# Performance work log

Hardware: AMD Instinct MI355X
Metric: run time of the kernel (lower is better)

## Reference

```python
import jax, jax.numpy as jnp
import numpy as np
import math

D_MODEL = 1024
DIM_K = 1024
DIM_V = 1024
N_HEADS = 16
B, T = 4, 1024


def setup_inputs() -> dict:
    key = jax.random.key(0)
    ks = jax.random.split(key, 12)
    s = 1.0 / math.sqrt(D_MODEL)
    inp = {
        "x": jax.random.normal(ks[0], (B, T, D_MODEL), jnp.float32),
        "mask": jax.random.randint(ks[1], (T, T), 0, 2, jnp.int32),
        "adj": jax.random.normal(ks[2], (T, T), jnp.float32) * 0.1,
        "Wq": jax.random.normal(ks[3], (D_MODEL, DIM_K), jnp.float32) * s,
        "bq": jnp.zeros((DIM_K,), jnp.float32),
        "Wk": jax.random.normal(ks[4], (D_MODEL, DIM_K), jnp.float32) * s,
        "bk": jnp.zeros((DIM_K,), jnp.float32),
        "Wv": jax.random.normal(ks[5], (D_MODEL, DIM_V), jnp.float32) * s,
        "bv": jnp.zeros((DIM_V,), jnp.float32),
        "Wo": jax.random.normal(ks[6], (DIM_V, D_MODEL), jnp.float32) * (1.0 / math.sqrt(DIM_V)),
        "bo": jnp.zeros((D_MODEL,), jnp.float32),
        "alpha": jnp.asarray(0.0, jnp.float32),
        "n_heads": N_HEADS,
    }
    return inp


def reference(x, mask, adj, Wq, bq, Wk, bk, Wv, bv, Wo, bo, alpha, n_heads):
    b, t, d = x.shape
    dim_k = Wq.shape[1]
    dim_v = Wv.shape[1]
    dkh = dim_k // n_heads
    dvh = dim_v // n_heads
    norm_fact = 1.0 / math.sqrt(dim_k)

    # torch .view(-1, B, T, dkh): plain row-major reshape with heads leading
    Q = (x @ Wq + bq).reshape(n_heads, b, t, dkh)
    K = (x @ Wk + bk).reshape(n_heads, b, t, dkh)
    V = (x @ Wv + bv).reshape(n_heads, b, t, dvh)

    # shared score computation [H, B, T, T]
    g_map = jnp.einsum("hbqd,hbkd->hbqk", Q, K) * norm_fact + adj
    l_map = jnp.where(mask == 0, jnp.asarray(-1e9, g_map.dtype), g_map)

    g_att = jax.nn.softmax(g_map, axis=-1)
    l_att = jax.nn.softmax(l_map, axis=-1)

    x_g = jnp.einsum("hbqk,hbkd->hbqd", g_att, V).reshape(b, t, -1)
    x_l = jnp.einsum("hbqk,hbkd->hbqd", l_att, V).reshape(b, t, -1)

    a = jax.nn.sigmoid(alpha)
    x_o = a * x_g + (1.0 - a) * x_l

    # signed sqrt + L2 normalize (norm=True)
    x_o = jnp.sqrt(jax.nn.relu(x_o)) - jnp.sqrt(jax.nn.relu(-x_o))
    x_o = x_o / jnp.maximum(jnp.linalg.norm(x_o, axis=-1, keepdims=True), 1e-12)

    return (x_o @ Wo + bo).reshape(-1, t, d)
```

## Files before the change

kernel.cpp:

```cpp
#include <hip/hip_runtime.h>
#include <hip/hip_bf16.h>


typedef __attribute__((ext_vector_type(8))) short short8;
typedef __attribute__((ext_vector_type(4))) float f32x4;
typedef __attribute__((ext_vector_type(2))) int i32x2;

__device__ __forceinline__ f32x4 mfma16(short8 a, short8 b, f32x4 c) {
  return __builtin_amdgcn_mfma_f32_16x16x32_bf16(a, b, c, 0, 0, 0);
}

__device__ __forceinline__ unsigned short f2b(float f) {
  __hip_bfloat16 h = __float2bfloat16(f);
  return *reinterpret_cast<unsigned short*>(&h);
}

__device__ __forceinline__ unsigned cvtpk(float lo, float hi) {
  unsigned r;
  asm("v_cvt_pk_bf16_f32 %0, %1, %2" : "=v"(r) : "v"(lo), "v"(hi));
  return r;
}

__device__ __forceinline__ float exp2h(float x) {
  float r;
  asm("v_exp_f32 %0, %1" : "=v"(r) : "v"(x));
  return r;
}

__device__ __forceinline__ unsigned ldsoff(const void* p) {
  return (unsigned)(size_t)(const __attribute__((address_space(3))) char*)p;
}

template <int OFF>
__device__ __forceinline__ i32x2 dstr(unsigned addr) {
  i32x2 d;
  asm volatile("ds_read_b64_tr_b16 %0, %1 offset:%c2"
               : "=v"(d) : "v"(addr), "i"(OFF) : "memory");
  return d;
}

__device__ __forceinline__ void gload_lds16(const void* g, void* l) {
  __builtin_amdgcn_global_load_lds(
      (const __attribute__((address_space(1))) void*)g,
      (__attribute__((address_space(3))) void*)l, 16, 0, 0);
}

__global__ __launch_bounds__(256) void k_cast_x(const float* __restrict__ x,
                                                unsigned short* __restrict__ xb) {
  int i = (blockIdx.x * 256 + threadIdx.x) * 8;
  float4 a = *reinterpret_cast<const float4*>(x + i);
  float4 b = *reinterpret_cast<const float4*>(x + i + 4);
  short8 o;
  o[0] = (short)f2b(a.x); o[1] = (short)f2b(a.y);
  o[2] = (short)f2b(a.z); o[3] = (short)f2b(a.w);
  o[4] = (short)f2b(b.x); o[5] = (short)f2b(b.y);
  o[6] = (short)f2b(b.z); o[7] = (short)f2b(b.w);
  *reinterpret_cast<short8*>(xb + i) = o;
}

__global__ __launch_bounds__(256) void k_transW(const float* __restrict__ Wq,
                                                const float* __restrict__ Wk,
                                                const float* __restrict__ Wv,
                                                const float* __restrict__ Wo,
                                                unsigned short* __restrict__ WcatT,
                                                unsigned short* __restrict__ WoT) {
  int wsel = blockIdx.z;
  const float* src = wsel == 0 ? Wq : wsel == 1 ? Wk : wsel == 2 ? Wv : Wo;
  unsigned short* dst = (wsel < 3) ? (WcatT + (size_t)wsel * 1024 * 1024) : WoT;
  int k0 = blockIdx.x * 64, n0 = blockIdx.y * 64;
  __shared__ float tile[64][65];
  int tr = threadIdx.x >> 6, tc = threadIdx.x & 63;
#pragma unroll
  for (int i = 0; i < 16; ++i) {
    int r = i * 4 + tr;
    tile[r][tc] = src[(size_t)(k0 + r) * 1024 + n0 + tc];
  }
  __syncthreads();
#pragma unroll
  for (int i = 0; i < 16; ++i) {
    int r = i * 4 + tr;
    dst[(size_t)(n0 + r) * 1024 + k0 + tc] = f2b(tile[tc][r]);
  }
}

__global__ __launch_bounds__(256) void k_pack(const float* __restrict__ adj,
                                              const int* __restrict__ mask,
                                              unsigned int* __restrict__ AM) {
  const float L2E = 1.4426950408889634f;
  int i = (blockIdx.x * 256 + threadIdx.x) * 4;
  int q = i >> 10, c = i & 1023;
  float4 a = *reinterpret_cast<const float4*>(adj + i);
  int4 m = *reinterpret_cast<const int4*>(mask + i);
  unsigned B = (unsigned)(q * 1024) + ((c >> 6) * 64) + ((c & 15) * 4) + ((c >> 4) & 3);
  AM[B]      = ((unsigned)f2b(a.x * L2E) << 16) | (m.x != 0 ? 1u : 0u);
  AM[B + 4]  = ((unsigned)f2b(a.y * L2E) << 16) | (m.y != 0 ? 1u : 0u);
  AM[B + 8]  = ((unsigned)f2b(a.z * L2E) << 16) | (m.z != 0 ? 1u : 0u);
  AM[B + 12] = ((unsigned)f2b(a.w * L2E) << 16) | (m.w != 0 ? 1u : 0u);
}

template <int MODE>
__global__ __launch_bounds__(256) void k_gemm(
    const unsigned short* __restrict__ A, const unsigned short* __restrict__ BT,
    float* __restrict__ outF,
    unsigned short* __restrict__ oQ, unsigned short* __restrict__ oK,
    unsigned short* __restrict__ oV,
    const float* __restrict__ b0, const float* __restrict__ b1,
    const float* __restrict__ b2, int M, int N, int K) {
  __shared__ unsigned short As[128 * 32], Bs[128 * 32];
  const int tid = threadIdx.x;
  const int w = tid >> 6, l = tid & 63, l15 = l & 15, l4 = l >> 4;
  const int m0 = blockIdx.x * 128, n0 = blockIdx.y * 128;
  const int wm = (w >> 1) * 64, wn = (w & 1) * 64;
  f32x4 acc[4][4];
#pragma unroll
  for (int i = 0; i < 4; ++i)
#pragma unroll
    for (int j = 0; j < 4; ++j) acc[i][j] = f32x4{0.f, 0.f, 0.f, 0.f};

  const int nkt = K >> 5;
  for (int kt = 0; kt < nkt; ++kt) {
#pragma unroll
    for (int i = 0; i < 2; ++i) {
      int c = i * 256 + tid;
      gload_lds16(A + (size_t)(m0 + (c >> 2)) * K + kt * 32 + (c & 3) * 8,
                  (char*)As + c * 16);
      gload_lds16(BT + (size_t)(n0 + (c >> 2)) * K + kt * 32 + (c & 3) * 8,
                  (char*)Bs + c * 16);
    }
    __syncthreads();
    short8 af[4], bf[4];
#pragma unroll
    for (int i = 0; i < 4; ++i)
      af[i] = *reinterpret_cast<const short8*>(As + (wm + i * 16 + l15) * 32 + l4 * 8);
#pragma unroll
    for (int j = 0; j < 4; ++j)
      bf[j] = *reinterpret_cast<const short8*>(Bs + (wn + j * 16 + l15) * 32 + l4 * 8);
#pragma unroll
    for (int i = 0; i < 4; ++i)
#pragma unroll
      for (int j = 0; j < 4; ++j) acc[i][j] = mfma16(af[i], bf[j], acc[i][j]);
    __syncthreads();
  }
#pragma unroll
  for (int i = 0; i < 4; ++i)
#pragma unroll
    for (int j = 0; j < 4; ++j) {
      int gr0 = m0 + wm + i * 16 + l4 * 4;
      int gc = n0 + wn + j * 16 + l15;
      if (MODE == 0) {
        int mat = gc >> 10, nl = gc & 1023;
        const float* bp = mat == 0 ? b0 : mat == 1 ? b1 : b2;
        unsigned short* op = mat == 0 ? oQ : mat == 1 ? oK : oV;
        float bb = bp[nl];
#pragma unroll
        for (int r = 0; r < 4; ++r)
          op[(size_t)(gr0 + r) * 1024 + nl] = f2b(acc[i][j][r] + bb);
      } else {
        float bb = b0[gc];
#pragma unroll
        for (int r = 0; r < 4; ++r)
          outF[(size_t)(gr0 + r) * N + gc] = acc[i][j][r] + bb;
      }
    }
}

__global__ __launch_bounds__(256) void k_attn(
    const unsigned short* __restrict__ Qb, const unsigned short* __restrict__ Kb,
    const unsigned short* __restrict__ Vb, const unsigned int* __restrict__ AM,
    float* __restrict__ Xg, float* __restrict__ Xl) {
  const int g = blockIdx.x;
  const int q0 = blockIdx.y * 64;
  const int tid = threadIdx.x;
  const int w = tid >> 6, l = tid & 63, l15 = l & 15, l4 = l >> 4;

  __shared__ unsigned short Kt[2][2][64][32];
  __shared__ unsigned short Vs[2][4][64][16];
  __shared__ unsigned short Pt[4][2][64][16];

  const size_t gbase = (size_t)g << 16;
  const unsigned short* Qg = Qb + gbase;
  const unsigned short* Kg = Kb + gbase;
  const unsigned short* Vg = Vb + gbase;

  short8 qf[2];
  {
    const unsigned short* qp = Qg + (size_t)(q0 + w * 16 + l15) * 64 + l4 * 8;
    qf[0] = *reinterpret_cast<const short8*>(qp);
    qf[1] = *reinterpret_cast<const short8*>(qp + 32);
  }
  short8 onesf;
#pragma unroll
  for (int j = 0; j < 8; ++j) onesf[j] = (short)0x3F80;

  f32x4 accg[4], accl[4];
#pragma unroll
  for (int d = 0; d < 4; ++d) {
    accg[d] = f32x4{0.f, 0.f, 0.f, 0.f};
    accl[d] = f32x4{0.f, 0.f, 0.f, 0.f};
  }
  f32x4 sumg = f32x4{0.f, 0.f, 0.f, 0.f}, suml = f32x4{0.f, 0.f, 0.f, 0.f};

  const int qrow = q0 + w * 16 + l4 * 4;
  const float NF2 = 0.04508422002778f;
  const uint4* AMr4 = (const uint4*)AM;
  const int kx8 = (l4 ^ ((l15 >> 1) & 3)) * 8;

  const unsigned ptw = ldsoff(&Pt[w][0][0][0]) + (unsigned)(l4 * 256 + l15 * 8);
  const unsigned vsb = ldsoff(&Vs[0][0][0][0]) + (unsigned)(l4 * 256 + l15 * 8);

  auto stage = [&](int b, int kk0) {
#pragma unroll
    for (int i = 0; i < 2; ++i) {
      int c = i * 256 + tid;
      int dk = c >> 8, key = (c >> 2) & 63, slot = c & 3;
      int ls = slot ^ ((key >> 1) & 3);
      gload_lds16(Kg + (size_t)(kk0 + key) * 64 + dk * 32 + ls * 8,
                  (char*)Kt + b * 8192 + c * 16);
    }
#pragma unroll
    for (int i = 0; i < 2; ++i) {
      int c = i * 256 + tid;
      int db = c >> 7, k = (c >> 1) & 63, h = c & 1;
      gload_lds16(Vg + (size_t)(kk0 + k) * 64 + db * 16 + h * 8,
                  (char*)Vs + b * 8192 + c * 16);
    }
  };

  stage(0, 0);
  __syncthreads();

  for (int kt = 0; kt < 16; ++kt) {
    const int b = kt & 1;
    if (kt < 15) stage(b ^ 1, (kt + 1) * 64);

    union { uint4 v; unsigned u[4]; } amu[4];
#pragma unroll
    for (int r = 0; r < 4; ++r)
      amu[r].v = AMr4[(size_t)(qrow + r) * 256 + kt * 16 + l15];

    f32x4 accs[4];
#pragma unroll
    for (int cb = 0; cb < 4; ++cb) accs[cb] = f32x4{0.f, 0.f, 0.f, 0.f};
#pragma unroll
    for (int cb = 0; cb < 4; ++cb)
#pragma unroll
      for (int dk = 0; dk < 2; ++dk)
        accs[cb] = mfma16(
            qf[dk],
            *reinterpret_cast<const short8*>(&Kt[b][dk][cb * 16 + l15][kx8]),
            accs[cb]);

#pragma unroll
    for (int cb = 0; cb < 4; ++cb) {
      unsigned am0 = amu[0].u[cb], am1 = amu[1].u[cb];
      unsigned am2 = amu[2].u[cb], am3 = amu[3].u[cb];
      float e0 = exp2h(fmaf(accs[cb][0], NF2, __uint_as_float(am0 & 0xffff0000u)));
      float e1 = exp2h(fmaf(accs[cb][1], NF2, __uint_as_float(am1 & 0xffff0000u)));
      float e2 = exp2h(fmaf(accs[cb][2], NF2, __uint_as_float(am2 & 0xffff0000u)));
      float e3 = exp2h(fmaf(accs[cb][3], NF2, __uint_as_float(am3 & 0xffff0000u)));
      float z0 = (am0 & 1u) ? e0 : 0.f;
      float z1 = (am1 & 1u) ? e1 : 0.f;
      float z2 = (am2 & 1u) ? e2 : 0.f;
      float z3 = (am3 & 1u) ? e3 : 0.f;
      int krow = cb * 16 + l15;
      *reinterpret_cast<uint2*>(&Pt[w][0][krow][l4 * 4]) =
          make_uint2(cvtpk(e0, e1), cvtpk(e2, e3));
      *reinterpret_cast<uint2*>(&Pt[w][1][krow][l4 * 4]) =
          make_uint2(cvtpk(z0, z1), cvtpk(z2, z3));
    }
    asm volatile("s_waitcnt lgkmcnt(0)" ::: "memory");

    const unsigned vb = vsb + (unsigned)(b << 13);
#pragma unroll
    for (int ks = 0; ks < 2; ++ks) {
      union { short8 s; i32x2 d[2]; } vf[4], pg, pl;
      if (ks == 0) {
#pragma unroll
        for (int db = 0; db < 4; ++db) {
          vf[db].d[0] = dstr<0 * 1024 + 0>(vb + db * 2048);
          vf[db].d[1] = dstr<0 * 1024 + 128>(vb + db * 2048);
        }
        pg.d[0] = dstr<0>(ptw);        pg.d[1] = dstr<128>(ptw);
        pl.d[0] = dstr<2048>(ptw);     pl.d[1] = dstr<2048 + 128>(ptw);
      } else {
#pragma unroll
        for (int db = 0; db < 4; ++db) {
          vf[db].d[0] = dstr<1 * 1024 + 0>(vb + db * 2048);
          vf[db].d[1] = dstr<1 * 1024 + 128>(vb + db * 2048);
        }
        pg.d[0] = dstr<1024>(ptw);     pg.d[1] = dstr<1024 + 128>(ptw);
        pl.d[0] = dstr<2048 + 1024>(ptw);
        pl.d[1] = dstr<2048 + 1024 + 128>(ptw);
      }
      asm volatile("s_waitcnt lgkmcnt(0)" ::: "memory");
      __builtin_amdgcn_sched_barrier(0);
#pragma unroll
      for (int db = 0; db < 4; ++db) {
        accg[db] = mfma16(pg.s, vf[db].s, accg[db]);
        accl[db] = mfma16(pl.s, vf[db].s, accl[db]);
      }
      sumg = mfma16(pg.s, onesf, sumg);
      suml = mfma16(pl.s, onesf, suml);
    }
    __syncthreads();
  }

#pragma unroll
  for (int r = 0; r < 4; ++r) {
    float ig = 1.f / sumg[r];
    float il = suml[r] > 0.f ? 1.f / suml[r] : 0.f;
#pragma unroll
    for (int db = 0; db < 4; ++db) {
      size_t o = gbase + (size_t)(qrow + r) * 64 + db * 16 + l15;
      Xg[o] = accg[db][r] * ig;
      Xl[o] = accl[db][r] * il;
    }
  }
}

__global__ __launch_bounds__(256) void k_combine(const float* __restrict__ Xg,
                                                 const float* __restrict__ Xl,
                                                 const float* __restrict__ alphap,
                                                 unsigned short* __restrict__ xob) {
  int row = blockIdx.x, tid = threadIdx.x;
  int w = tid >> 6, l = tid & 63;
  size_t base = (size_t)row * 1024 + tid * 4;
  float a = 1.f / (1.f + __expf(-alphap[0]));
  float4 gx = *reinterpret_cast<const float4*>(Xg + base);
  float4 lx = *reinterpret_cast<const float4*>(Xl + base);
  float v[4];
  {
    float t0 = a * gx.x + (1.f - a) * lx.x;
    float t1 = a * gx.y + (1.f - a) * lx.y;
    float t2 = a * gx.z + (1.f - a) * lx.z;
    float t3 = a * gx.w + (1.f - a) * lx.w;
    v[0] = t0 >= 0.f ? sqrtf(t0) : -sqrtf(-t0);
    v[1] = t1 >= 0.f ? sqrtf(t1) : -sqrtf(-t1);
    v[2] = t2 >= 0.f ? sqrtf(t2) : -sqrtf(-t2);
    v[3] = t3 >= 0.f ? sqrtf(t3) : -sqrtf(-t3);
  }
  float ss = v[0] * v[0] + v[1] * v[1] + v[2] * v[2] + v[3] * v[3];
#pragma unroll
  for (int off = 1; off < 64; off <<= 1) ss += __shfl_xor(ss, off);
  __shared__ float wsum[4];
  if (l == 0) wsum[w] = ss;
  __syncthreads();
  float tot = wsum[0] + wsum[1] + wsum[2] + wsum[3];
  float scale = 1.f / fmaxf(sqrtf(tot), 1e-12f);
  ushort4 o;
  o.x = f2b(v[0] * scale); o.y = f2b(v[1] * scale);
  o.z = f2b(v[2] * scale); o.w = f2b(v[3] * scale);
  *reinterpret_cast<ushort4*>(xob + base) = o;
}

extern "C" void kernel_launch(void* const* d_in, const int* in_sizes, int n_in,
                              void* d_out, int out_size, void* d_ws, size_t ws_size,
                              hipStream_t stream) {
  const float* x     = (const float*)d_in[0];
  const int*   mask  = (const int*)d_in[1];
  const float* adj   = (const float*)d_in[2];
  const float* Wq    = (const float*)d_in[3];
  const float* bq    = (const float*)d_in[4];
  const float* Wk    = (const float*)d_in[5];
  const float* bk    = (const float*)d_in[6];
  const float* Wv    = (const float*)d_in[7];
  const float* bv    = (const float*)d_in[8];
  const float* Wo    = (const float*)d_in[9];
  const float* bo    = (const float*)d_in[10];
  const float* alpha = (const float*)d_in[11];
  float* out = (float*)d_out;
  char* ws = (char*)d_ws;

  unsigned short* xb    = (unsigned short*)(ws + 0);
  unsigned short* WcatT = (unsigned short*)(ws + 8388608);
  unsigned short* WoT   = (unsigned short*)(ws + 14680064);
  unsigned short* Qb    = (unsigned short*)(ws + 16777216);
  unsigned short* Kb    = (unsigned short*)(ws + 25165824);
  unsigned short* Vb    = (unsigned short*)(ws + 33554432);
  float*          Xg    = (float*)(ws + 41943040);
  float*          Xl    = (float*)(ws + 58720256);
  unsigned short* xob   = (unsigned short*)(ws + 75497472);
  unsigned int*   AM    = (unsigned int*)(ws + 83886080);

  k_cast_x<<<2048, 256, 0, stream>>>(x, xb);
  k_transW<<<dim3(16, 16, 4), 256, 0, stream>>>(Wq, Wk, Wv, Wo, WcatT, WoT);
  k_pack<<<1024, 256, 0, stream>>>(adj, mask, AM);
  k_gemm<0><<<dim3(32, 24), 256, 0, stream>>>(xb, WcatT, nullptr, Qb, Kb, Vb,
                                              bq, bk, bv, 4096, 3072, 1024);
  k_attn<<<dim3(64, 16), 256, 0, stream>>>(Qb, Kb, Vb, AM, Xg, Xl);
  k_combine<<<4096, 256, 0, stream>>>(Xg, Xl, alpha, xob);
  k_gemm<1><<<dim3(32, 8), 256, 0, stream>>>(xob, WoT, out, nullptr, nullptr,
                                             nullptr, bo, bo, bo, 4096, 1024, 1024);
}
```

Baseline: 234.9 us.

## Process two query sub-tiles per wave in attention to reuse staged K/V

Each attention block now covers 128 query rows instead of 64, with every wave handling two 16-row sub-tiles. K fragments are loaded into registers once and reused across both sub-tiles, and each staged K/V tile serves twice as many queries. This halves global K/V traffic and staging work per query, at the cost of more registers, fewer blocks (512 instead of 1024), and a serialized reuse of the shared Pt buffer between the sub-tiles. launch_bounds is set to 2 blocks per SIMD-group to cap register growth.

```diff
diff --git a/kernel.cpp b/kernel.cpp
--- a/kernel.cpp
+++ b/kernel.cpp
@@ -164,12 +164,12 @@
     }
 }
 
-__global__ __launch_bounds__(256) void k_attn(
+__global__ __launch_bounds__(256, 2) void k_attn(
     const unsigned short* __restrict__ Qb, const unsigned short* __restrict__ Kb,
     const unsigned short* __restrict__ Vb, const unsigned int* __restrict__ AM,
     float* __restrict__ Xg, float* __restrict__ Xl) {
   const int g = blockIdx.x;
-  const int q0 = blockIdx.y * 64;
+  const int q0 = blockIdx.y * 128;
   const int tid = threadIdx.x;
   const int w = tid >> 6, l = tid & 63, l15 = l & 15, l4 = l >> 4;
 
@@ -182,25 +182,31 @@
   const unsigned short* Kg = Kb + gbase;
   const unsigned short* Vg = Vb + gbase;
 
-  short8 qf[2];
-  {
-    const unsigned short* qp = Qg + (size_t)(q0 + w * 16 + l15) * 64 + l4 * 8;
-    qf[0] = *reinterpret_cast<const short8*>(qp);
-    qf[1] = *reinterpret_cast<const short8*>(qp + 32);
+  short8 qf[2][2];
+#pragma unroll
+  for (int s = 0; s < 2; ++s) {
+    const unsigned short* qp =
+        Qg + (size_t)(q0 + w * 32 + s * 16 + l15) * 64 + l4 * 8;
+    qf[s][0] = *reinterpret_cast<const short8*>(qp);
+    qf[s][1] = *reinterpret_cast<const short8*>(qp + 32);
   }
   short8 onesf;
 #pragma unroll
   for (int j = 0; j < 8; ++j) onesf[j] = (short)0x3F80;
 
-  f32x4 accg[4], accl[4];
-#pragma unroll
-  for (int d = 0; d < 4; ++d) {
-    accg[d] = f32x4{0.f, 0.f, 0.f, 0.f};
-    accl[d] = f32x4{0.f, 0.f, 0.f, 0.f};
-  }
-  f32x4 sumg = f32x4{0.f, 0.f, 0.f, 0.f}, suml = f32x4{0.f, 0.f, 0.f, 0.f};
-
-  const int qrow = q0 + w * 16 + l4 * 4;
+  f32x4 accg[2][4], accl[2][4], sumg[2], suml[2];
+#pragma unroll
+  for (int s = 0; s < 2; ++s) {
+    sumg[s] = f32x4{0.f, 0.f, 0.f, 0.f};
+    suml[s] = f32x4{0.f, 0.f, 0.f, 0.f};
+#pragma unroll
+    for (int d = 0; d < 4; ++d) {
+      accg[s][d] = f32x4{0.f, 0.f, 0.f, 0.f};
+      accl[s][d] = f32x4{0.f, 0.f, 0.f, 0.f};
+    }
+  }
+
+  const int qrowb = q0 + w * 32 + l4 * 4;
   const float NF2 = 0.04508422002778f;
   const uint4* AMr4 = (const uint4*)AM;
   const int kx8 = (l4 ^ ((l15 >> 1) & 3)) * 8;
@@ -233,89 +239,104 @@
     const int b = kt & 1;
     if (kt < 15) stage(b ^ 1, (kt + 1) * 64);
 
-    union { uint4 v; unsigned u[4]; } amu[4];
-#pragma unroll
-    for (int r = 0; r < 4; ++r)
-      amu[r].v = AMr4[(size_t)(qrow + r) * 256 + kt * 16 + l15];
-
-    f32x4 accs[4];
-#pragma unroll
-    for (int cb = 0; cb < 4; ++cb) accs[cb] = f32x4{0.f, 0.f, 0.f, 0.f};
+    short8 kf[4][2];
 #pragma unroll
     for (int cb = 0; cb < 4; ++cb)
 #pragma unroll
       for (int dk = 0; dk < 2; ++dk)
-        accs[cb] = mfma16(
-            qf[dk],
-            *reinterpret_cast<const short8*>(&Kt[b][dk][cb * 16 + l15][kx8]),
-            accs[cb]);
-
-#pragma unroll
-    for (int cb = 0; cb < 4; ++cb) {
-      unsigned am0 = amu[0].u[cb], am1 = amu[1].u[cb];
-      unsigned am2 = amu[2].u[cb], am3 = amu[3].u[cb];
-      float e0 = exp2h(fmaf(accs[cb][0], NF2, __uint_as_float(am0 & 0xffff0000u)));
-      float e1 = exp2h(fmaf(accs[cb][1], NF2, __uint_as_float(am1 & 0xffff0000u)));
-      float e2 = exp2h(fmaf(accs[cb][2], NF2, __uint_as_float(am2 & 0xffff0000u)));
-      float e3 = exp2h(fmaf(accs[cb][3], NF2, __uint_as_float(am3 & 0xffff0000u)));
-      float z0 = (am0 & 1u) ? e0 : 0.f;
-      float z1 = (am1 & 1u) ? e1 : 0.f;
-      float z2 = (am2 & 1u) ? e2 : 0.f;
-      float z3 = (am3 & 1u) ? e3 : 0.f;
-      int krow = cb * 16 + l15;
-      *reinterpret_cast<uint2*>(&Pt[w][0][krow][l4 * 4]) =
-          make_uint2(cvtpk(e0, e1), cvtpk(e2, e3));
-      *reinterpret_cast<uint2*>(&Pt[w][1][krow][l4 * 4]) =
-          make_uint2(cvtpk(z0, z1), cvtpk(z2, z3));
-    }
-    asm volatile("s_waitcnt lgkmcnt(0)" ::: "memory");
+        kf[cb][dk] =
+            *reinterpret_cast<const short8*>(&Kt[b][dk][cb * 16 + l15][kx8]);
+
+    f32x4 accs[2][4];
+#pragma unroll
+    for (int s = 0; s < 2; ++s)
+#pragma unroll
+      for (int cb = 0; cb < 4; ++cb) accs[s][cb] = f32x4{0.f, 0.f, 0.f, 0.f};
+#pragma unroll
+    for (int cb = 0; cb < 4; ++cb)
+#pragma unroll
+      for (int s = 0; s < 2; ++s)
+#pragma unroll
+        for (int dk = 0; dk < 2; ++dk)
+          accs[s][cb] = mfma16(qf[s][dk], kf[cb][dk], accs[s][cb]);
 
     const unsigned vb = vsb + (unsigned)(b << 13);
-#pragma unroll
-    for (int ks = 0; ks < 2; ++ks) {
-      union { short8 s; i32x2 d[2]; } vf[4], pg, pl;
-      if (ks == 0) {
-#pragma unroll
-        for (int db = 0; db < 4; ++db) {
-          vf[db].d[0] = dstr<0 * 1024 + 0>(vb + db * 2048);
-          vf[db].d[1] = dstr<0 * 1024 + 128>(vb + db * 2048);
-        }
-        pg.d[0] = dstr<0>(ptw);        pg.d[1] = dstr<128>(ptw);
-        pl.d[0] = dstr<2048>(ptw);     pl.d[1] = dstr<2048 + 128>(ptw);
-      } else {
-#pragma unroll
-        for (int db = 0; db < 4; ++db) {
-          vf[db].d[0] = dstr<1 * 1024 + 0>(vb + db * 2048);
-          vf[db].d[1] = dstr<1 * 1024 + 128>(vb + db * 2048);
-        }
-        pg.d[0] = dstr<1024>(ptw);     pg.d[1] = dstr<1024 + 128>(ptw);
-        pl.d[0] = dstr<2048 + 1024>(ptw);
-        pl.d[1] = dstr<2048 + 1024 + 128>(ptw);
+
+#pragma unroll
+    for (int s = 0; s < 2; ++s) {
+      union { uint4 v; unsigned u[4]; } amu[4];
+#pragma unroll
+      for (int r = 0; r < 4; ++r)
+        amu[r].v = AMr4[(size_t)(qrowb + s * 16 + r) * 256 + kt * 16 + l15];
+
+#pragma unroll
+      for (int cb = 0; cb < 4; ++cb) {
+        unsigned am0 = amu[0].u[cb], am1 = amu[1].u[cb];
+        unsigned am2 = amu[2].u[cb], am3 = amu[3].u[cb];
+        float e0 = exp2h(fmaf(accs[s][cb][0], NF2, __uint_as_float(am0 & 0xffff0000u)));
+        float e1 = exp2h(fmaf(accs[s][cb][1], NF2, __uint_as_float(am1 & 0xffff0000u)));
+        float e2 = exp2h(fmaf(accs[s][cb][2], NF2, __uint_as_float(am2 & 0xffff0000u)));
+        float e3 = exp2h(fmaf(accs[s][cb][3], NF2, __uint_as_float(am3 & 0xffff0000u)));
+        float z0 = (am0 & 1u) ? e0 : 0.f;
+        float z1 = (am1 & 1u) ? e1 : 0.f;
+        float z2 = (am2 & 1u) ? e2 : 0.f;
+        float z3 = (am3 & 1u) ? e3 : 0.f;
+        int krow = cb * 16 + l15;
+        *reinterpret_cast<uint2*>(&Pt[w][0][krow][l4 * 4]) =
+            make_uint2(cvtpk(e0, e1), cvtpk(e2, e3));
+        *reinterpret_cast<uint2*>(&Pt[w][1][krow][l4 * 4]) =
+            make_uint2(cvtpk(z0, z1), cvtpk(z2, z3));
       }
       asm volatile("s_waitcnt lgkmcnt(0)" ::: "memory");
-      __builtin_amdgcn_sched_barrier(0);
+
+#pragma unroll
+      for (int ks = 0; ks < 2; ++ks) {
+        union { short8 s8; i32x2 d[2]; } vf[4], pg, pl;
+        if (ks == 0) {
+#pragma unroll
+          for (int db = 0; db < 4; ++db) {
+            vf[db].d[0] = dstr<0>(vb + db * 2048);
+            vf[db].d[1] = dstr<128>(vb + db * 2048);
+          }
+          pg.d[0] = dstr<0>(ptw);        pg.d[1] = dstr<128>(ptw);
+          pl.d[0] = dstr<2048>(ptw);     pl.d[1] = dstr<2048 + 128>(ptw);
+        } else {
+#pragma unroll
+          for (int db = 0; db < 4; ++db) {
+            vf[db].d[0] = dstr<1024>(vb + db * 2048);
+            vf[db].d[1] = dstr<1024 + 128>(vb + db * 2048);
+          }
+          pg.d[0] = dstr<1024>(ptw);     pg.d[1] = dstr<1024 + 128>(ptw);
+          pl.d[0] = dstr<2048 + 1024>(ptw);
+          pl.d[1] = dstr<2048 + 1024 + 128>(ptw);
+        }
+        asm volatile("s_waitcnt lgkmcnt(0)" ::: "memory");
+        __builtin_amdgcn_sched_barrier(0);
+#pragma unroll
+        for (int db = 0; db < 4; ++db) {
+          accg[s][db] = mfma16(pg.s8, vf[db].s8, accg[s][db]);
+          accl[s][db] = mfma16(pl.s8, vf[db].s8, accl[s][db]);
+        }
+        sumg[s] = mfma16(pg.s8, onesf, sumg[s]);
+        suml[s] = mfma16(pl.s8, onesf, suml[s]);
+      }
+    }
+    __syncthreads();
+  }
+
+#pragma unroll
+  for (int s = 0; s < 2; ++s)
+#pragma unroll
+    for (int r = 0; r < 4; ++r) {
+      float ig = 1.f / sumg[s][r];
+      float il = suml[s][r] > 0.f ? 1.f / suml[s][r] : 0.f;
 #pragma unroll
       for (int db = 0; db < 4; ++db) {
-        accg[db] = mfma16(pg.s, vf[db].s, accg[db]);
-        accl[db] = mfma16(pl.s, vf[db].s, accl[db]);
+        size_t o = gbase + (size_t)(qrowb + s * 16 + r) * 64 + db * 16 + l15;
+        Xg[o] = accg[s][db][r] * ig;
+        Xl[o] = accl[s][db][r] * il;
       }
-      sumg = mfma16(pg.s, onesf, sumg);
-      suml = mfma16(pl.s, onesf, suml);
-    }
-    __syncthreads();
-  }
-
-#pragma unroll
-  for (int r = 0; r < 4; ++r) {
-    float ig = 1.f / sumg[r];
-    float il = suml[r] > 0.f ? 1.f / suml[r] : 0.f;
-#pragma unroll
-    for (int db = 0; db < 4; ++db) {
-      size_t o = gbase + (size_t)(qrow + r) * 64 + db * 16 + l15;
-      Xg[o] = accg[db][r] * ig;
-      Xl[o] = accl[db][r] * il;
-    }
-  }
+    }
 }
 
 __global__ __launch_bounds__(256) void k_combine(const float* __restrict__ Xg,
@@ -387,7 +408,7 @@
   k_pack<<<1024, 256, 0, stream>>>(adj, mask, AM);
   k_gemm<0><<<dim3(32, 24), 256, 0, stream>>>(xb, WcatT, nullptr, Qb, Kb, Vb,
                                               bq, bk, bv, 4096, 3072, 1024);
-  k_attn<<<dim3(64, 16), 256, 0, stream>>>(Qb, Kb, Vb, AM, Xg, Xl);
+  k_attn<<<dim3(64, 8), 256, 0, stream>>>(Qb, Kb, Vb, AM, Xg, Xl);
   k_combine<<<4096, 256, 0, stream>>>(Xg, Xl, alpha, xob);
   k_gemm<1><<<dim3(32, 8), 256, 0, stream>>>(xob, WoT, out, nullptr, nullptr,
                                              nullptr, bo, bo, bo, 4096, 1024, 1024);
```

Result: no change. 232.0 us (-1.2%).

## Keep attention probabilities in registers via transposed QK^T and permuted key order

Applied to the files above, without the earlier changes.

The QK^T MFMA is computed with operands swapped, S^T = K·Q^T. The keys feeding each lane are permuted so the score fragment can be packed straight into bf16 A-operands for the PV MFMA, which removes the per-warp Pt LDS round trip (write, wait, read back). The adj/mask pack kernel writes a new tiled layout so each lane fetches its bias/mask words with contiguous uint4 loads, and the K LDS swizzle is extended to suit the new access pattern. Launch bounds request 4 blocks per CU and the key loop is unrolled by two, which could raise register pressure or cause spills.

```diff
diff --git a/kernel.cpp b/kernel.cpp
--- a/kernel.cpp
+++ b/kernel.cpp
@@ -91,11 +91,14 @@
   int q = i >> 10, c = i & 1023;
   float4 a = *reinterpret_cast<const float4*>(adj + i);
   int4 m = *reinterpret_cast<const int4*>(mask + i);
-  unsigned B = (unsigned)(q * 1024) + ((c >> 6) * 64) + ((c & 15) * 4) + ((c >> 4) & 3);
-  AM[B]      = ((unsigned)f2b(a.x * L2E) << 16) | (m.x != 0 ? 1u : 0u);
-  AM[B + 4]  = ((unsigned)f2b(a.y * L2E) << 16) | (m.y != 0 ? 1u : 0u);
-  AM[B + 8]  = ((unsigned)f2b(a.z * L2E) << 16) | (m.z != 0 ? 1u : 0u);
-  AM[B + 12] = ((unsigned)f2b(a.w * L2E) << 16) | (m.w != 0 ? 1u : 0u);
+  int kt = c >> 6, h = (c >> 5) & 1, g = (c >> 3) & 3, e0 = c & 7;
+  unsigned W = (unsigned)((kt * 8 + h * 4 + g) * 8192 + q * 8 + e0);
+  uint4 o;
+  o.x = ((unsigned)f2b(a.x * L2E) << 16) | (m.x != 0 ? 1u : 0u);
+  o.y = ((unsigned)f2b(a.y * L2E) << 16) | (m.y != 0 ? 1u : 0u);
+  o.z = ((unsigned)f2b(a.z * L2E) << 16) | (m.z != 0 ? 1u : 0u);
+  o.w = ((unsigned)f2b(a.w * L2E) << 16) | (m.w != 0 ? 1u : 0u);
+  *reinterpret_cast<uint4*>(AM + W) = o;
 }
 
 template <int MODE>
@@ -164,7 +167,7 @@
     }
 }
 
-__global__ __launch_bounds__(256) void k_attn(
+__global__ __launch_bounds__(256, 4) void k_attn(
     const unsigned short* __restrict__ Qb, const unsigned short* __restrict__ Kb,
     const unsigned short* __restrict__ Vb, const unsigned int* __restrict__ AM,
     float* __restrict__ Xg, float* __restrict__ Xl) {
@@ -175,7 +178,6 @@
 
   __shared__ unsigned short Kt[2][2][64][32];
   __shared__ unsigned short Vs[2][4][64][16];
-  __shared__ unsigned short Pt[4][2][64][16];
 
   const size_t gbase = (size_t)g << 16;
   const unsigned short* Qg = Qb + gbase;
@@ -200,20 +202,27 @@
   }
   f32x4 sumg = f32x4{0.f, 0.f, 0.f, 0.f}, suml = f32x4{0.f, 0.f, 0.f, 0.f};
 
+  const float NF2 = 0.04508422002778f;
+  const int q_abs = q0 + w * 16 + l15;
   const int qrow = q0 + w * 16 + l4 * 4;
-  const float NF2 = 0.04508422002778f;
-  const uint4* AMr4 = (const uint4*)AM;
-  const int kx8 = (l4 ^ ((l15 >> 1) & 3)) * 8;
-
-  const unsigned ptw = ldsoff(&Pt[w][0][0][0]) + (unsigned)(l4 * 256 + l15 * 8);
+
+  int koff[4];
+#pragma unroll
+  for (int cb = 0; cb < 4; ++cb) {
+    int key = 8 * (l15 >> 2) + (l15 & 3) + 4 * (cb & 1) + 32 * (cb >> 1);
+    int sl = l4 ^ (((key >> 1) ^ (key >> 3)) & 3);
+    koff[cb] = key * 64 + sl * 16;
+  }
+  const unsigned ktb = ldsoff(&Kt[0][0][0][0]);
   const unsigned vsb = ldsoff(&Vs[0][0][0][0]) + (unsigned)(l4 * 256 + l15 * 8);
+  const unsigned* AMq = AM + (size_t)q_abs * 8;
 
   auto stage = [&](int b, int kk0) {
 #pragma unroll
     for (int i = 0; i < 2; ++i) {
       int c = i * 256 + tid;
       int dk = c >> 8, key = (c >> 2) & 63, slot = c & 3;
-      int ls = slot ^ ((key >> 1) & 3);
+      int ls = slot ^ (((key >> 1) ^ (key >> 3)) & 3);
       gload_lds16(Kg + (size_t)(kk0 + key) * 64 + dk * 32 + ls * 8,
                   (char*)Kt + b * 8192 + c * 16);
     }
@@ -229,79 +238,91 @@
   stage(0, 0);
   __syncthreads();
 
+#pragma unroll 2
   for (int kt = 0; kt < 16; ++kt) {
     const int b = kt & 1;
     if (kt < 15) stage(b ^ 1, (kt + 1) * 64);
 
-    union { uint4 v; unsigned u[4]; } amu[4];
-#pragma unroll
-    for (int r = 0; r < 4; ++r)
-      amu[r].v = AMr4[(size_t)(qrow + r) * 256 + kt * 16 + l15];
+    union { uint4 v; unsigned u[4]; } amc[4];
+    {
+      const unsigned* p0 = AMq + (size_t)(kt * 8 + l4) * 8192;
+      const unsigned* p1 = AMq + (size_t)(kt * 8 + 4 + l4) * 8192;
+      amc[0].v = *reinterpret_cast<const uint4*>(p0);
+      amc[1].v = *reinterpret_cast<const uint4*>(p0 + 4);
+      amc[2].v = *reinterpret_cast<const uint4*>(p1);
+      amc[3].v = *reinterpret_cast<const uint4*>(p1 + 4);
+    }
 
     f32x4 accs[4];
 #pragma unroll
-    for (int cb = 0; cb < 4; ++cb) accs[cb] = f32x4{0.f, 0.f, 0.f, 0.f};
-#pragma unroll
-    for (int cb = 0; cb < 4; ++cb)
-#pragma unroll
-      for (int dk = 0; dk < 2; ++dk)
-        accs[cb] = mfma16(
-            qf[dk],
-            *reinterpret_cast<const short8*>(&Kt[b][dk][cb * 16 + l15][kx8]),
-            accs[cb]);
-
-#pragma unroll
     for (int cb = 0; cb < 4; ++cb) {
-      unsigned am0 = amu[0].u[cb], am1 = amu[1].u[cb];
-      unsigned am2 = amu[2].u[cb], am3 = amu[3].u[cb];
-      float e0 = exp2h(fmaf(accs[cb][0], NF2, __uint_as_float(am0 & 0xffff0000u)));
-      float e1 = exp2h(fmaf(accs[cb][1], NF2, __uint_as_float(am1 & 0xffff0000u)));
-      float e2 = exp2h(fmaf(accs[cb][2], NF2, __uint_as_float(am2 & 0xffff0000u)));
-      float e3 = exp2h(fmaf(accs[cb][3], NF2, __uint_as_float(am3 & 0xffff0000u)));
-      float z0 = (am0 & 1u) ? e0 : 0.f;
-      float z1 = (am1 & 1u) ? e1 : 0.f;
-      float z2 = (am2 & 1u) ? e2 : 0.f;
-      float z3 = (am3 & 1u) ? e3 : 0.f;
-      int krow = cb * 16 + l15;
-      *reinterpret_cast<uint2*>(&Pt[w][0][krow][l4 * 4]) =
-          make_uint2(cvtpk(e0, e1), cvtpk(e2, e3));
-      *reinterpret_cast<uint2*>(&Pt[w][1][krow][l4 * 4]) =
-          make_uint2(cvtpk(z0, z1), cvtpk(z2, z3));
-    }
+      accs[cb] = f32x4{0.f, 0.f, 0.f, 0.f};
+#pragma unroll
+      for (int dk = 0; dk < 2; ++dk) {
+        short8 kf = *reinterpret_cast<const short8*>(
+            (const char*)Kt + b * 8192 + dk * 4096 + koff[cb]);
+        accs[cb] = mfma16(kf, qf[dk], accs[cb]);
+      }
+    }
+
+    const unsigned vb = vsb + (unsigned)(b << 13);
+    union { short8 s8; i32x2 d[2]; } vf[4];
+#pragma unroll
+    for (int db = 0; db < 4; ++db) {
+      vf[db].d[0] = dstr<0>(vb + db * 2048);
+      vf[db].d[1] = dstr<128>(vb + db * 2048);
+    }
+
+    unsigned pgq[8], plq[8];
+#pragma unroll
+    for (int cb = 0; cb < 4; ++cb) {
+      unsigned a0 = amc[cb].u[0], a1 = amc[cb].u[1];
+      unsigned a2 = amc[cb].u[2], a3 = amc[cb].u[3];
+      float e0 = exp2h(fmaf(accs[cb][0], NF2, __uint_as_float(a0 & 0xffff0000u)));
+      float e1 = exp2h(fmaf(accs[cb][1], NF2, __uint_as_float(a1 & 0xffff0000u)));
+      float e2 = exp2h(fmaf(accs[cb][2], NF2, __uint_as_float(a2 & 0xffff0000u)));
+      float e3 = exp2h(fmaf(accs[cb][3], NF2, __uint_as_float(a3 & 0xffff0000u)));
+      float z0 = (a0 & 1u) ? e0 : 0.f;
+      float z1 = (a1 & 1u) ? e1 : 0.f;
+      float z2 = (a2 & 1u) ? e2 : 0.f;
+      float z3 = (a3 & 1u) ? e3 : 0.f;
+      pgq[cb * 2]     = cvtpk(e0, e1);
+      pgq[cb * 2 + 1] = cvtpk(e2, e3);
+      plq[cb * 2]     = cvtpk(z0, z1);
+      plq[cb * 2 + 1] = cvtpk(z2, z3);
+    }
+    union { short8 s8; unsigned u[4]; } pg0, pl0, pg1, pl1;
+#pragma unroll
+    for (int v = 0; v < 4; ++v) {
+      pg0.u[v] = pgq[v];     pl0.u[v] = plq[v];
+      pg1.u[v] = pgq[4 + v]; pl1.u[v] = plq[4 + v];
+    }
+
     asm volatile("s_waitcnt lgkmcnt(0)" ::: "memory");
-
-    const unsigned vb = vsb + (unsigned)(b << 13);
-#pragma unroll
-    for (int ks = 0; ks < 2; ++ks) {
-      union { short8 s; i32x2 d[2]; } vf[4], pg, pl;
-      if (ks == 0) {
-#pragma unroll
-        for (int db = 0; db < 4; ++db) {
-          vf[db].d[0] = dstr<0 * 1024 + 0>(vb + db * 2048);
-          vf[db].d[1] = dstr<0 * 1024 + 128>(vb + db * 2048);
-        }
-        pg.d[0] = dstr<0>(ptw);        pg.d[1] = dstr<128>(ptw);
-        pl.d[0] = dstr<2048>(ptw);     pl.d[1] = dstr<2048 + 128>(ptw);
-      } else {
-#pragma unroll
-        for (int db = 0; db < 4; ++db) {
-          vf[db].d[0] = dstr<1 * 1024 + 0>(vb + db * 2048);
-          vf[db].d[1] = dstr<1 * 1024 + 128>(vb + db * 2048);
-        }
-        pg.d[0] = dstr<1024>(ptw);     pg.d[1] = dstr<1024 + 128>(ptw);
-        pl.d[0] = dstr<2048 + 1024>(ptw);
-        pl.d[1] = dstr<2048 + 1024 + 128>(ptw);
-      }
-      asm volatile("s_waitcnt lgkmcnt(0)" ::: "memory");
-      __builtin_amdgcn_sched_barrier(0);
-#pragma unroll
-      for (int db = 0; db < 4; ++db) {
-        accg[db] = mfma16(pg.s, vf[db].s, accg[db]);
-        accl[db] = mfma16(pl.s, vf[db].s, accl[db]);
-      }
-      sumg = mfma16(pg.s, onesf, sumg);
-      suml = mfma16(pl.s, onesf, suml);
-    }
+    __builtin_amdgcn_sched_barrier(0);
+#pragma unroll
+    for (int db = 0; db < 4; ++db) {
+      accg[db] = mfma16(pg0.s8, vf[db].s8, accg[db]);
+      accl[db] = mfma16(pl0.s8, vf[db].s8, accl[db]);
+    }
+    sumg = mfma16(pg0.s8, onesf, sumg);
+    suml = mfma16(pl0.s8, onesf, suml);
+
+#pragma unroll
+    for (int db = 0; db < 4; ++db) {
+      vf[db].d[0] = dstr<1024>(vb + db * 2048);
+      vf[db].d[1] = dstr<1024 + 128>(vb + db * 2048);
+    }
+    asm volatile("s_waitcnt lgkmcnt(0)" ::: "memory");
+    __builtin_amdgcn_sched_barrier(0);
+#pragma unroll
+    for (int db = 0; db < 4; ++db) {
+      accg[db] = mfma16(pg1.s8, vf[db].s8, accg[db]);
+      accl[db] = mfma16(pl1.s8, vf[db].s8, accl[db]);
+    }
+    sumg = mfma16(pg1.s8, onesf, sumg);
+    suml = mfma16(pl1.s8, onesf, suml);
+
     __syncthreads();
   }
 
```

Result: no change. 230.5 us (-1.9%).
